# Performance work log

Measured on AMD Instinct MI355X. Metric: run time of the kernel, lower is better.

The kernel has to match this reference:

```python
import jax, jax.numpy as jnp
import numpy as np

B, N, C, H = 2, 2048, 1024, 16
HD = C // H  # head dim = 64


def setup_inputs() -> dict:
    key = jax.random.key(0)
    kq, kk, kv, km = jax.random.split(key, 4)
    q = jax.random.normal(kq, (B, N, C), dtype=jnp.float32)
    k = jax.random.normal(kk, (B, N, C), dtype=jnp.float32)
    v = jax.random.normal(kv, (B, N, C), dtype=jnp.float32)
    mask = jax.random.randint(km, (B, 1, N, N), 0, 2, dtype=jnp.int32)
    return {"q": q, "k": k, "v": v, "mask": mask}


def reference(q, k, v, mask):
    b, n, c = q.shape
    # (B, N, C) -> (B, H, N, HD)
    qh = q.reshape(b, n, H, HD).transpose(0, 2, 1, 3)
    kh = k.reshape(b, n, H, HD).transpose(0, 2, 1, 3)
    vh = v.reshape(b, n, H, HD).transpose(0, 2, 1, 3)
    scale = 1.0 / jnp.sqrt(jnp.float32(HD))
    # scores: (B, H, N, N)
    scores = jnp.einsum("bhqd,bhkd->bhqk", qh, kh) * scale
    scores = jnp.where(mask == 0, jnp.float32(-1e9), scores)
    probs = jax.nn.softmax(scores, axis=-1)
    atten = jnp.einsum("bhqk,bhkd->bhqd", probs, vh)
    # (B, H, N, HD) -> (B, N, C)
    return atten.transpose(0, 2, 1, 3).reshape(b, n, c)
```

## Files before the change

kernel.cpp:

```cpp
#include <hip/hip_runtime.h>
#include <hip/hip_bf16.h>

#define B_ 2
#define N_ 2048
#define C_ 1024
#define H_ 16
#define HD_ 64

#define KT 64
#define KSTR 72
#define VSTR 72
#define PSTR 72
#define NW 8
#define QB 128

typedef short s16x8 __attribute__((ext_vector_type(8)));
typedef short s16x4 __attribute__((ext_vector_type(4)));
typedef float f32x4 __attribute__((ext_vector_type(4)));

__device__ __forceinline__ ushort f2bf(float x) {
    __hip_bfloat16 h = __float2bfloat16(x);
    return *reinterpret_cast<ushort*>(&h);
}

__device__ __forceinline__ s16x8 cvt8(float4 a, float4 b) {
    union { s16x8 v; __hip_bfloat162 h[4]; } u;
    u.h[0] = __float22bfloat162_rn(float2{a.x, a.y});
    u.h[1] = __float22bfloat162_rn(float2{a.z, a.w});
    u.h[2] = __float22bfloat162_rn(float2{b.x, b.y});
    u.h[3] = __float22bfloat162_rn(float2{b.z, b.w});
    return u.v;
}

__global__ __launch_bounds__(256)
void pack_mask(const int* __restrict__ M, unsigned long long* __restrict__ bits) {
    const int gw   = (blockIdx.x * 256 + threadIdx.x) >> 6;
    const int lane = threadIdx.x & 63;
#pragma unroll
    for (int it = 0; it < 16; ++it) {
        const size_t wi = (size_t)gw * 16 + it;
        unsigned long long bal = __ballot(M[wi * 64 + lane] != 0);
        if (lane == 0) bits[wi] = bal;
    }
}

__global__ __launch_bounds__(512)
void mha_fwd(const float* __restrict__ Q, const float* __restrict__ K,
             const float* __restrict__ V, const unsigned* __restrict__ bits,
             float* __restrict__ O) {
    __shared__ ushort Kl[KT * KSTR];
    __shared__ ushort Vt[HD_ * VSTR];
    __shared__ ushort Pl[NW][16 * PSTR];

    const int qt   = blockIdx.x;
    const int h    = blockIdx.y;
    const int b    = blockIdx.z;
    const int tid  = threadIdx.x;
    const int w    = tid >> 6;
    const int lane = tid & 63;
    const int l16  = lane & 15;
    const int quad = lane >> 4;

    const size_t head_off = (size_t)b * N_ * C_ + (size_t)h * HD_;
    const int qb = qt * QB + w * 16;

    const float qs = 0.125f * 1.44269504088896f;
    const size_t qoff = head_off + (size_t)(qb + l16) * C_ + quad * 8;
    float4 q0 = *(const float4*)(Q + qoff);
    float4 q1 = *(const float4*)(Q + qoff + 4);
    float4 q2 = *(const float4*)(Q + qoff + 32);
    float4 q3 = *(const float4*)(Q + qoff + 36);
    q0.x*=qs; q0.y*=qs; q0.z*=qs; q0.w*=qs;
    q1.x*=qs; q1.y*=qs; q1.z*=qs; q1.w*=qs;
    q2.x*=qs; q2.y*=qs; q2.z*=qs; q2.w*=qs;
    q3.x*=qs; q3.y*=qs; q3.z*=qs; q3.w*=qs;
    const s16x8 qa0 = cvt8(q0, q1);
    const s16x8 qa1 = cvt8(q2, q3);

    f32x4 acc[4];
#pragma unroll
    for (int c = 0; c < 4; ++c) acc[c] = f32x4{0.f, 0.f, 0.f, 0.f};
    float lsum = 0.f;

    const int skey = tid >> 3;
    const int sd0  = (tid & 7) * 8;
    const int vcol = (skey & 7) | ((((skey >> 3) ^ (tid & 7)) & 7) << 3);

    const unsigned* brow = bits + ((size_t)b * N_ + qb + l16) * (N_ / 32);

    const float SHIFT = 16.0f;

    for (int kt = 0; kt < N_ / KT; ++kt) {
        __syncthreads();
        {
            const size_t kbase = head_off + (size_t)(kt * KT + skey) * C_ + sd0;
            float4 k0 = *(const float4*)(K + kbase);
            float4 k1 = *(const float4*)(K + kbase + 4);
            *(s16x8*)(&Kl[skey * KSTR + sd0]) = cvt8(k0, k1);
            float4 v0 = *(const float4*)(V + kbase);
            float4 v1 = *(const float4*)(V + kbase + 4);
            const float* vp = (const float*)&v0;
#pragma unroll
            for (int i = 0; i < 4; ++i)
                Vt[(sd0 + i) * VSTR + vcol] = f2bf(vp[i]);
            const float* vq = (const float*)&v1;
#pragma unroll
            for (int i = 0; i < 4; ++i)
                Vt[(sd0 + 4 + i) * VSTR + vcol] = f2bf(vq[i]);
        }
        const unsigned w0 = brow[2 * kt];
        const unsigned w1 = brow[2 * kt + 1];
        __syncthreads();

        f32x4 s[4];
#pragma unroll
        for (int t = 0; t < 4; ++t) {
            s16x8 kb0 = *(const s16x8*)(&Kl[(t * 16 + l16) * KSTR + quad * 8]);
            s16x8 kb1 = *(const s16x8*)(&Kl[(t * 16 + l16) * KSTR + quad * 8 + 32]);
            f32x4 z = {0.f, 0.f, 0.f, 0.f};
            z = __builtin_amdgcn_mfma_f32_16x16x32_bf16(kb0, qa0, z, 0, 0, 0);
            z = __builtin_amdgcn_mfma_f32_16x16x32_bf16(kb1, qa1, z, 0, 0, 0);
            s[t] = z;
        }

        const unsigned a0 = w0 >> (quad * 4);
        const unsigned a1 = w1 >> (quad * 4);
#pragma unroll
        for (int t = 0; t < 4; ++t) {
            const unsigned aw = (t < 2) ? a0 : a1;
            const int sh = (t & 1) * 16;
            float p0 = exp2f((((aw >> (sh + 0)) & 1u) ? s[t][0] : -1e9f) - SHIFT);
            float p1 = exp2f((((aw >> (sh + 1)) & 1u) ? s[t][1] : -1e9f) - SHIFT);
            float p2 = exp2f((((aw >> (sh + 2)) & 1u) ? s[t][2] : -1e9f) - SHIFT);
            float p3 = exp2f((((aw >> (sh + 3)) & 1u) ? s[t][3] : -1e9f) - SHIFT);
            lsum += (p0 + p1) + (p2 + p3);
            union { s16x4 v; __hip_bfloat162 h[2]; } u;
            u.h[0] = __float22bfloat162_rn(float2{p0, p1});
            u.h[1] = __float22bfloat162_rn(float2{p2, p3});
            *(s16x4*)(&Pl[w][l16 * PSTR + t * 16 + quad * 4]) = u.v;
        }

#pragma unroll
        for (int half = 0; half < 2; ++half) {
            s16x8 pa = *(const s16x8*)(&Pl[w][l16 * PSTR + half * 32 + quad * 8]);
#pragma unroll
            for (int c = 0; c < 4; ++c) {
                const int dr  = c * 16 + l16;
                const int blk = (half * 4 + quad) ^ ((dr >> 3) & 7);
                s16x8 vb = *(const s16x8*)(&Vt[dr * VSTR + blk * 8]);
                acc[c] = __builtin_amdgcn_mfma_f32_16x16x32_bf16(pa, vb, acc[c], 0, 0, 0);
            }
        }
    }

    lsum += __shfl_xor(lsum, 16);
    lsum += __shfl_xor(lsum, 32);

#pragma unroll
    for (int r = 0; r < 4; ++r) {
        const float inv = 1.0f / __shfl(lsum, quad * 4 + r);
        const size_t obase = head_off + (size_t)(qb + quad * 4 + r) * C_;
        O[obase + l16]      = acc[0][r] * inv;
        O[obase + l16 + 16] = acc[1][r] * inv;
        O[obase + l16 + 32] = acc[2][r] * inv;
        O[obase + l16 + 48] = acc[3][r] * inv;
    }
}

extern "C" void kernel_launch(void* const* d_in, const int* in_sizes, int n_in,
                              void* d_out, int out_size, void* d_ws, size_t ws_size,
                              hipStream_t stream) {
    const float* q = (const float*)d_in[0];
    const float* k = (const float*)d_in[1];
    const float* v = (const float*)d_in[2];
    const int*   m = (const int*)d_in[3];
    float*       o = (float*)d_out;

    hipLaunchKernelGGL(pack_mask, dim3(2048), dim3(256), 0, stream,
                       m, (unsigned long long*)d_ws);

    dim3 grid(N_ / QB, H_, B_);
    hipLaunchKernelGGL(mha_fwd, grid, dim3(512), 0, stream,
                       q, k, v, (const unsigned*)d_ws, o);
}
```

Measured before the change: 194.4 us.

## Give each wave two 16-row query groups and halve block size to 256 threads

Each wave now handles 32 query rows as two 16-row groups. Every K and V fragment read from LDS feeds two MFMAs, so LDS reads per FLOP are halved. The block shrinks to 4 waves with launch bounds of 2 blocks per CU, and staging is rebalanced: each thread loads 16 K elements and converts V rows in pairs into packed 32-bit transposed LDS stores. In exchange, each wave holds twice the accumulators and score registers, which could pressure occupancy, and there are fewer threads to hide global-load latency.

```diff
diff --git a/kernel.cpp b/kernel.cpp
--- a/kernel.cpp
+++ b/kernel.cpp
@@ -11,7 +11,7 @@
 #define KSTR 72
 #define VSTR 72
 #define PSTR 72
-#define NW 8
+#define NW 4
 #define QB 128
 
 typedef short s16x8 __attribute__((ext_vector_type(8)));
@@ -44,13 +44,13 @@
     }
 }
 
-__global__ __launch_bounds__(512)
+__global__ __launch_bounds__(256, 2)
 void mha_fwd(const float* __restrict__ Q, const float* __restrict__ K,
              const float* __restrict__ V, const unsigned* __restrict__ bits,
              float* __restrict__ O) {
     __shared__ ushort Kl[KT * KSTR];
     __shared__ ushort Vt[HD_ * VSTR];
-    __shared__ ushort Pl[NW][16 * PSTR];
+    __shared__ ushort Pl[NW][32 * PSTR];
 
     const int qt   = blockIdx.x;
     const int h    = blockIdx.y;
@@ -62,31 +62,40 @@
     const int quad = lane >> 4;
 
     const size_t head_off = (size_t)b * N_ * C_ + (size_t)h * HD_;
-    const int qb = qt * QB + w * 16;
+    const int qb = qt * QB + w * 32;
 
     const float qs = 0.125f * 1.44269504088896f;
-    const size_t qoff = head_off + (size_t)(qb + l16) * C_ + quad * 8;
-    float4 q0 = *(const float4*)(Q + qoff);
-    float4 q1 = *(const float4*)(Q + qoff + 4);
-    float4 q2 = *(const float4*)(Q + qoff + 32);
-    float4 q3 = *(const float4*)(Q + qoff + 36);
-    q0.x*=qs; q0.y*=qs; q0.z*=qs; q0.w*=qs;
-    q1.x*=qs; q1.y*=qs; q1.z*=qs; q1.w*=qs;
-    q2.x*=qs; q2.y*=qs; q2.z*=qs; q2.w*=qs;
-    q3.x*=qs; q3.y*=qs; q3.z*=qs; q3.w*=qs;
-    const s16x8 qa0 = cvt8(q0, q1);
-    const s16x8 qa1 = cvt8(q2, q3);
-
-    f32x4 acc[4];
-#pragma unroll
-    for (int c = 0; c < 4; ++c) acc[c] = f32x4{0.f, 0.f, 0.f, 0.f};
-    float lsum = 0.f;
-
-    const int skey = tid >> 3;
-    const int sd0  = (tid & 7) * 8;
-    const int vcol = (skey & 7) | ((((skey >> 3) ^ (tid & 7)) & 7) << 3);
-
-    const unsigned* brow = bits + ((size_t)b * N_ + qb + l16) * (N_ / 32);
+    s16x8 qa[2][2];
+#pragma unroll
+    for (int g = 0; g < 2; ++g) {
+        const size_t qoff = head_off + (size_t)(qb + g * 16 + l16) * C_ + quad * 8;
+        float4 q0 = *(const float4*)(Q + qoff);
+        float4 q1 = *(const float4*)(Q + qoff + 4);
+        float4 q2 = *(const float4*)(Q + qoff + 32);
+        float4 q3 = *(const float4*)(Q + qoff + 36);
+        q0.x*=qs; q0.y*=qs; q0.z*=qs; q0.w*=qs;
+        q1.x*=qs; q1.y*=qs; q1.z*=qs; q1.w*=qs;
+        q2.x*=qs; q2.y*=qs; q2.z*=qs; q2.w*=qs;
+        q3.x*=qs; q3.y*=qs; q3.z*=qs; q3.w*=qs;
+        qa[g][0] = cvt8(q0, q1);
+        qa[g][1] = cvt8(q2, q3);
+    }
+
+    f32x4 acc[2][4];
+#pragma unroll
+    for (int g = 0; g < 2; ++g)
+#pragma unroll
+        for (int c = 0; c < 4; ++c) acc[g][c] = f32x4{0.f, 0.f, 0.f, 0.f};
+    float lsum[2] = {0.f, 0.f};
+
+    const int skey = tid >> 2;
+    const int sd0  = (tid & 3) * 16;
+    const int kp   = tid >> 3;
+    const int vd0  = (tid & 7) * 8;
+    const int vcol = (2 * (kp & 3)) | ((((kp >> 2) ^ (tid & 7)) & 7) << 3);
+
+    const unsigned* brow0 = bits + ((size_t)b * N_ + qb + l16) * (N_ / 32);
+    const unsigned* brow1 = brow0 + (size_t)16 * (N_ / 32);
 
     const float SHIFT = 16.0f;
 
@@ -96,74 +105,102 @@
             const size_t kbase = head_off + (size_t)(kt * KT + skey) * C_ + sd0;
             float4 k0 = *(const float4*)(K + kbase);
             float4 k1 = *(const float4*)(K + kbase + 4);
-            *(s16x8*)(&Kl[skey * KSTR + sd0]) = cvt8(k0, k1);
-            float4 v0 = *(const float4*)(V + kbase);
-            float4 v1 = *(const float4*)(V + kbase + 4);
-            const float* vp = (const float*)&v0;
-#pragma unroll
-            for (int i = 0; i < 4; ++i)
-                Vt[(sd0 + i) * VSTR + vcol] = f2bf(vp[i]);
-            const float* vq = (const float*)&v1;
-#pragma unroll
-            for (int i = 0; i < 4; ++i)
-                Vt[(sd0 + 4 + i) * VSTR + vcol] = f2bf(vq[i]);
-        }
-        const unsigned w0 = brow[2 * kt];
-        const unsigned w1 = brow[2 * kt + 1];
+            float4 k2 = *(const float4*)(K + kbase + 8);
+            float4 k3 = *(const float4*)(K + kbase + 12);
+            *(s16x8*)(&Kl[skey * KSTR + sd0])     = cvt8(k0, k1);
+            *(s16x8*)(&Kl[skey * KSTR + sd0 + 8]) = cvt8(k2, k3);
+
+            const size_t vbase = head_off + (size_t)(kt * KT + 2 * kp) * C_ + vd0;
+            float4 a0 = *(const float4*)(V + vbase);
+            float4 a1 = *(const float4*)(V + vbase + 4);
+            float4 b0 = *(const float4*)(V + vbase + C_);
+            float4 b1 = *(const float4*)(V + vbase + C_ + 4);
+            const float* ap = (const float*)&a0;
+            const float* bp = (const float*)&b0;
+#pragma unroll
+            for (int i = 0; i < 4; ++i) {
+                __hip_bfloat162 pr = __float22bfloat162_rn(float2{ap[i], bp[i]});
+                *(unsigned*)(&Vt[(vd0 + i) * VSTR + vcol]) = *(unsigned*)&pr;
+            }
+            const float* aq = (const float*)&a1;
+            const float* bq = (const float*)&b1;
+#pragma unroll
+            for (int i = 0; i < 4; ++i) {
+                __hip_bfloat162 pr = __float22bfloat162_rn(float2{aq[i], bq[i]});
+                *(unsigned*)(&Vt[(vd0 + 4 + i) * VSTR + vcol]) = *(unsigned*)&pr;
+            }
+        }
+        const unsigned m00 = brow0[2 * kt];
+        const unsigned m01 = brow0[2 * kt + 1];
+        const unsigned m10 = brow1[2 * kt];
+        const unsigned m11 = brow1[2 * kt + 1];
         __syncthreads();
 
-        f32x4 s[4];
+        f32x4 s[2][4];
 #pragma unroll
         for (int t = 0; t < 4; ++t) {
             s16x8 kb0 = *(const s16x8*)(&Kl[(t * 16 + l16) * KSTR + quad * 8]);
             s16x8 kb1 = *(const s16x8*)(&Kl[(t * 16 + l16) * KSTR + quad * 8 + 32]);
-            f32x4 z = {0.f, 0.f, 0.f, 0.f};
-            z = __builtin_amdgcn_mfma_f32_16x16x32_bf16(kb0, qa0, z, 0, 0, 0);
-            z = __builtin_amdgcn_mfma_f32_16x16x32_bf16(kb1, qa1, z, 0, 0, 0);
-            s[t] = z;
-        }
-
-        const unsigned a0 = w0 >> (quad * 4);
-        const unsigned a1 = w1 >> (quad * 4);
-#pragma unroll
-        for (int t = 0; t < 4; ++t) {
-            const unsigned aw = (t < 2) ? a0 : a1;
-            const int sh = (t & 1) * 16;
-            float p0 = exp2f((((aw >> (sh + 0)) & 1u) ? s[t][0] : -1e9f) - SHIFT);
-            float p1 = exp2f((((aw >> (sh + 1)) & 1u) ? s[t][1] : -1e9f) - SHIFT);
-            float p2 = exp2f((((aw >> (sh + 2)) & 1u) ? s[t][2] : -1e9f) - SHIFT);
-            float p3 = exp2f((((aw >> (sh + 3)) & 1u) ? s[t][3] : -1e9f) - SHIFT);
-            lsum += (p0 + p1) + (p2 + p3);
-            union { s16x4 v; __hip_bfloat162 h[2]; } u;
-            u.h[0] = __float22bfloat162_rn(float2{p0, p1});
-            u.h[1] = __float22bfloat162_rn(float2{p2, p3});
-            *(s16x4*)(&Pl[w][l16 * PSTR + t * 16 + quad * 4]) = u.v;
+#pragma unroll
+            for (int g = 0; g < 2; ++g) {
+                f32x4 z = {0.f, 0.f, 0.f, 0.f};
+                z = __builtin_amdgcn_mfma_f32_16x16x32_bf16(kb0, qa[g][0], z, 0, 0, 0);
+                z = __builtin_amdgcn_mfma_f32_16x16x32_bf16(kb1, qa[g][1], z, 0, 0, 0);
+                s[g][t] = z;
+            }
+        }
+
+#pragma unroll
+        for (int g = 0; g < 2; ++g) {
+            const unsigned a0 = (g ? m10 : m00) >> (quad * 4);
+            const unsigned a1 = (g ? m11 : m01) >> (quad * 4);
+#pragma unroll
+            for (int t = 0; t < 4; ++t) {
+                const unsigned aw = (t < 2) ? a0 : a1;
+                const int sh = (t & 1) * 16;
+                float p0 = exp2f((((aw >> (sh + 0)) & 1u) ? s[g][t][0] : -1e9f) - SHIFT);
+                float p1 = exp2f((((aw >> (sh + 1)) & 1u) ? s[g][t][1] : -1e9f) - SHIFT);
+                float p2 = exp2f((((aw >> (sh + 2)) & 1u) ? s[g][t][2] : -1e9f) - SHIFT);
+                float p3 = exp2f((((aw >> (sh + 3)) & 1u) ? s[g][t][3] : -1e9f) - SHIFT);
+                lsum[g] += (p0 + p1) + (p2 + p3);
+                union { s16x4 v; __hip_bfloat162 h[2]; } u;
+                u.h[0] = __float22bfloat162_rn(float2{p0, p1});
+                u.h[1] = __float22bfloat162_rn(float2{p2, p3});
+                *(s16x4*)(&Pl[w][(g * 16 + l16) * PSTR + t * 16 + quad * 4]) = u.v;
+            }
         }
 
 #pragma unroll
         for (int half = 0; half < 2; ++half) {
-            s16x8 pa = *(const s16x8*)(&Pl[w][l16 * PSTR + half * 32 + quad * 8]);
+            s16x8 pa0 = *(const s16x8*)(&Pl[w][(l16)      * PSTR + half * 32 + quad * 8]);
+            s16x8 pa1 = *(const s16x8*)(&Pl[w][(16 + l16) * PSTR + half * 32 + quad * 8]);
 #pragma unroll
             for (int c = 0; c < 4; ++c) {
                 const int dr  = c * 16 + l16;
                 const int blk = (half * 4 + quad) ^ ((dr >> 3) & 7);
                 s16x8 vb = *(const s16x8*)(&Vt[dr * VSTR + blk * 8]);
-                acc[c] = __builtin_amdgcn_mfma_f32_16x16x32_bf16(pa, vb, acc[c], 0, 0, 0);
-            }
-        }
-    }
-
-    lsum += __shfl_xor(lsum, 16);
-    lsum += __shfl_xor(lsum, 32);
-
-#pragma unroll
-    for (int r = 0; r < 4; ++r) {
-        const float inv = 1.0f / __shfl(lsum, quad * 4 + r);
-        const size_t obase = head_off + (size_t)(qb + quad * 4 + r) * C_;
-        O[obase + l16]      = acc[0][r] * inv;
-        O[obase + l16 + 16] = acc[1][r] * inv;
-        O[obase + l16 + 32] = acc[2][r] * inv;
-        O[obase + l16 + 48] = acc[3][r] * inv;
+                acc[0][c] = __builtin_amdgcn_mfma_f32_16x16x32_bf16(pa0, vb, acc[0][c], 0, 0, 0);
+                acc[1][c] = __builtin_amdgcn_mfma_f32_16x16x32_bf16(pa1, vb, acc[1][c], 0, 0, 0);
+            }
+        }
+    }
+
+#pragma unroll
+    for (int g = 0; g < 2; ++g) {
+        lsum[g] += __shfl_xor(lsum[g], 16);
+        lsum[g] += __shfl_xor(lsum[g], 32);
+    }
+#pragma unroll
+    for (int g = 0; g < 2; ++g) {
+#pragma unroll
+        for (int r = 0; r < 4; ++r) {
+            const float inv = 1.0f / __shfl(lsum[g], quad * 4 + r);
+            const size_t obase = head_off + (size_t)(qb + g * 16 + quad * 4 + r) * C_;
+            O[obase + l16]      = acc[g][0][r] * inv;
+            O[obase + l16 + 16] = acc[g][1][r] * inv;
+            O[obase + l16 + 32] = acc[g][2][r] * inv;
+            O[obase + l16 + 48] = acc[g][3][r] * inv;
+        }
     }
 }
 
@@ -180,6 +217,6 @@
                        m, (unsigned long long*)d_ws);
 
     dim3 grid(N_ / QB, H_, B_);
-    hipLaunchKernelGGL(mha_fwd, grid, dim3(512), 0, stream,
+    hipLaunchKernelGGL(mha_fwd, grid, dim3(256), 0, stream,
                        q, k, v, (const unsigned*)d_ws, o);
 }
```

New measurement: 210.4 us. +8.2%, slower.

## Double-buffer K/V LDS tiles with register prefetch and paired V transpose stores

Applied to the files above, without the earlier changes.

K/V tiles now sit in two LDS buffers. The next tile's global loads are issued into registers before the current tile's compute and written to the alternate buffer afterwards, so one barrier per iteration suffices and load latency overlaps the MFMA work. The V transpose is reorganised so each thread converts two adjacent keys and writes a packed 32-bit pair, halving the scalar LDS stores. Launch bounds now request four blocks per CU. This adds LDS use and register pressure, which may limit occupancy or cause spills.

```diff
diff --git a/kernel.cpp b/kernel.cpp
--- a/kernel.cpp
+++ b/kernel.cpp
@@ -8,6 +8,7 @@
 #define HD_ 64
 
 #define KT 64
+#define NT (N_ / KT)
 #define KSTR 72
 #define VSTR 72
 #define PSTR 72
@@ -17,11 +18,6 @@
 typedef short s16x8 __attribute__((ext_vector_type(8)));
 typedef short s16x4 __attribute__((ext_vector_type(4)));
 typedef float f32x4 __attribute__((ext_vector_type(4)));
-
-__device__ __forceinline__ ushort f2bf(float x) {
-    __hip_bfloat16 h = __float2bfloat16(x);
-    return *reinterpret_cast<ushort*>(&h);
-}
 
 __device__ __forceinline__ s16x8 cvt8(float4 a, float4 b) {
     union { s16x8 v; __hip_bfloat162 h[4]; } u;
@@ -44,12 +40,12 @@
     }
 }
 
-__global__ __launch_bounds__(512)
+__global__ __launch_bounds__(512, 4)
 void mha_fwd(const float* __restrict__ Q, const float* __restrict__ K,
              const float* __restrict__ V, const unsigned* __restrict__ bits,
              float* __restrict__ O) {
-    __shared__ ushort Kl[KT * KSTR];
-    __shared__ ushort Vt[HD_ * VSTR];
+    __shared__ ushort Kl[2][KT * KSTR];
+    __shared__ ushort Vt[2][HD_ * VSTR];
     __shared__ ushort Pl[NW][16 * PSTR];
 
     const int qt   = blockIdx.x;
@@ -84,39 +80,53 @@
 
     const int skey = tid >> 3;
     const int sd0  = (tid & 7) * 8;
-    const int vcol = (skey & 7) | ((((skey >> 3) ^ (tid & 7)) & 7) << 3);
+    const int kp   = tid >> 4;
+    const int vd0  = (tid & 15) * 4;
+    const int vcol = 2 * (kp & 3) + ((((kp >> 2) ^ (vd0 >> 3)) & 7) << 3);
 
     const unsigned* brow = bits + ((size_t)b * N_ + qb + l16) * (N_ / 32);
 
     const float SHIFT = 16.0f;
 
-    for (int kt = 0; kt < N_ / KT; ++kt) {
-        __syncthreads();
-        {
-            const size_t kbase = head_off + (size_t)(kt * KT + skey) * C_ + sd0;
-            float4 k0 = *(const float4*)(K + kbase);
-            float4 k1 = *(const float4*)(K + kbase + 4);
-            *(s16x8*)(&Kl[skey * KSTR + sd0]) = cvt8(k0, k1);
-            float4 v0 = *(const float4*)(V + kbase);
-            float4 v1 = *(const float4*)(V + kbase + 4);
-            const float* vp = (const float*)&v0;
-#pragma unroll
-            for (int i = 0; i < 4; ++i)
-                Vt[(sd0 + i) * VSTR + vcol] = f2bf(vp[i]);
-            const float* vq = (const float*)&v1;
-#pragma unroll
-            for (int i = 0; i < 4; ++i)
-                Vt[(sd0 + 4 + i) * VSTR + vcol] = f2bf(vq[i]);
+    {
+        const size_t kbase = head_off + (size_t)(skey) * C_ + sd0;
+        float4 kA = *(const float4*)(K + kbase);
+        float4 kB = *(const float4*)(K + kbase + 4);
+        *(s16x8*)(&Kl[0][skey * KSTR + sd0]) = cvt8(kA, kB);
+        const size_t vbase = head_off + (size_t)(2 * kp) * C_ + vd0;
+        float4 vA = *(const float4*)(V + vbase);
+        float4 vB = *(const float4*)(V + vbase + C_);
+        const float* ap = (const float*)&vA;
+        const float* bp = (const float*)&vB;
+#pragma unroll
+        for (int i = 0; i < 4; ++i) {
+            __hip_bfloat162 pr = __float22bfloat162_rn(float2{ap[i], bp[i]});
+            *(unsigned*)(&Vt[0][(vd0 + i) * VSTR + vcol]) = *(unsigned*)&pr;
+        }
+    }
+
+    for (int kt = 0; kt < NT; ++kt) {
+        const int cur = kt & 1;
+        float4 kA, kB, vA, vB;
+        const bool has_next = (kt + 1 < NT);
+        if (has_next) {
+            const size_t kbase = head_off + (size_t)((kt + 1) * KT + skey) * C_ + sd0;
+            kA = *(const float4*)(K + kbase);
+            kB = *(const float4*)(K + kbase + 4);
+            const size_t vbase = head_off + (size_t)((kt + 1) * KT + 2 * kp) * C_ + vd0;
+            vA = *(const float4*)(V + vbase);
+            vB = *(const float4*)(V + vbase + C_);
         }
         const unsigned w0 = brow[2 * kt];
         const unsigned w1 = brow[2 * kt + 1];
+
         __syncthreads();
 
         f32x4 s[4];
 #pragma unroll
         for (int t = 0; t < 4; ++t) {
-            s16x8 kb0 = *(const s16x8*)(&Kl[(t * 16 + l16) * KSTR + quad * 8]);
-            s16x8 kb1 = *(const s16x8*)(&Kl[(t * 16 + l16) * KSTR + quad * 8 + 32]);
+            s16x8 kb0 = *(const s16x8*)(&Kl[cur][(t * 16 + l16) * KSTR + quad * 8]);
+            s16x8 kb1 = *(const s16x8*)(&Kl[cur][(t * 16 + l16) * KSTR + quad * 8 + 32]);
             f32x4 z = {0.f, 0.f, 0.f, 0.f};
             z = __builtin_amdgcn_mfma_f32_16x16x32_bf16(kb0, qa0, z, 0, 0, 0);
             z = __builtin_amdgcn_mfma_f32_16x16x32_bf16(kb1, qa1, z, 0, 0, 0);
@@ -147,8 +157,19 @@
             for (int c = 0; c < 4; ++c) {
                 const int dr  = c * 16 + l16;
                 const int blk = (half * 4 + quad) ^ ((dr >> 3) & 7);
-                s16x8 vb = *(const s16x8*)(&Vt[dr * VSTR + blk * 8]);
+                s16x8 vb = *(const s16x8*)(&Vt[cur][dr * VSTR + blk * 8]);
                 acc[c] = __builtin_amdgcn_mfma_f32_16x16x32_bf16(pa, vb, acc[c], 0, 0, 0);
+            }
+        }
+
+        if (has_next) {
+            *(s16x8*)(&Kl[1 - cur][skey * KSTR + sd0]) = cvt8(kA, kB);
+            const float* ap = (const float*)&vA;
+            const float* bp = (const float*)&vB;
+#pragma unroll
+            for (int i = 0; i < 4; ++i) {
+                __hip_bfloat162 pr = __float22bfloat162_rn(float2{ap[i], bp[i]});
+                *(unsigned*)(&Vt[1 - cur][(vd0 + i) * VSTR + vcol]) = *(unsigned*)&pr;
             }
         }
     }
```

Result: no change. 195.0 us (+0.3%).
